# Kernel tuning notes

Hardware: AMD Instinct MI355X
Metric: run time of the kernel (lower is better)

## Reference

```python
import jax, jax.numpy as jnp
from jax import lax
import numpy as np

B, GRID, H = 128, 28, 64      # batch, 28x28 pixel grid, hidden size
NDIR = 4                      # feature_sz = number of scan directions
FC_HD, OUT = 512, 10


def setup_inputs() -> dict:
    key = jax.random.key(0)
    ks = jax.random.split(key, 8)
    s_u = 1.0 / np.sqrt(2 * H)
    inp = {
        "x":  jax.random.normal(ks[0], (B, GRID, GRID), dtype=jnp.float32),
        # per-direction MDLSTM gate params: 5 gates (i, f_left, f_up, o, g)
        "Wx": jax.random.normal(ks[1], (NDIR, 5 * H), dtype=jnp.float32) * 0.1,
        "U":  jax.random.normal(ks[2], (NDIR, 2 * H, 5 * H), dtype=jnp.float32) * s_u,
        "b":  jnp.zeros((NDIR, 5 * H), dtype=jnp.float32),
        # fc head
        "W1": jax.random.normal(ks[3], (NDIR * H, FC_HD), dtype=jnp.float32) / np.sqrt(NDIR * H),
        "b1": jnp.zeros((FC_HD,), dtype=jnp.float32),
        "W2": jax.random.normal(ks[4], (FC_HD, OUT), dtype=jnp.float32) / np.sqrt(FC_HD),
        "b2": jnp.zeros((OUT,), dtype=jnp.float32),
    }
    return inp


def _mdlstm_dir(xg, Wx, U, b):
    # xg: [GRID(rows), GRID(cols), B] scalar pixel per cell
    zeros = jnp.zeros((xg.shape[-1], H), dtype=xg.dtype)

    def col_step(carry, inp):
        h_left, c_left = carry
        x_pix, h_up, c_up = inp                     # [B], [B,H], [B,H]
        z = x_pix[:, None] * Wx + jnp.concatenate([h_left, h_up], -1) @ U + b
        i, f1, f2, o, g = jnp.split(z, 5, axis=-1)  # each [B,H]
        c = (jax.nn.sigmoid(i) * jnp.tanh(g)
             + jax.nn.sigmoid(f1) * c_left
             + jax.nn.sigmoid(f2) * c_up)
        h = jax.nn.sigmoid(o) * jnp.tanh(c)
        return (h, c), (h, c)

    def row_step(carry, x_row):
        h_up_row, c_up_row = carry                  # [GRID,B,H] previous row
        _, (h_row, c_row) = lax.scan(col_step, (zeros, zeros),
                                     (x_row, h_up_row, c_up_row))
        return (h_row, c_row), None

    init = (jnp.zeros((GRID,) + zeros.shape, xg.dtype),
            jnp.zeros((GRID,) + zeros.shape, xg.dtype))
    (h_last_row, _), _ = lax.scan(row_step, init, xg)
    return h_last_row[-1]                           # final (bottom-right) hidden [B,H]


def _forward(x, Wx, U, b, W1, b1, W2, b2):
    x2 = x.reshape(-1, GRID, GRID)
    # 4 scan directions via flips; scan always proceeds top-left -> bottom-right
    dirs = jnp.stack([x2,
                      x2[:, :, ::-1],
                      x2[:, ::-1, :],
                      x2[:, ::-1, ::-1]], 0)        # [4,B,GRID,GRID]
    dirs = jnp.transpose(dirs, (0, 2, 3, 1))        # [4,GRID,GRID,B]
    h = jax.vmap(_mdlstm_dir)(dirs, Wx, U, b)       # [4,B,H]
    h = jnp.transpose(h, (1, 0, 2)).reshape(-1, NDIR * H)
    z = jax.nn.relu(h @ W1 + b1)
    return jax.nn.softmax(z @ W2 + b2, axis=-1)


def reference(x, Wx, U, b, W1, b1, W2, b2):
    return _forward(x, Wx, U, b, W1, b1, W2, b2)
```

## Files before the change

kernel.cpp:

```cpp
#include <hip/hip_runtime.h>
#include <hip/hip_bf16.h>


#define GRIDN 28
#define BATCH 128
#define HID   64
#define NDIR  4
#define FC_HD 512
#define OUT_N 10
#define BT    2
#define NTHR  768
#define NSLOT 29
#define S_H   104
#define S_C   68

typedef _Float16 f16;
typedef _Float16 f16x8 __attribute__((ext_vector_type(8)));
typedef float    f32x4 __attribute__((ext_vector_type(4)));

__device__ __forceinline__ float sigf(float x) {
    return __builtin_amdgcn_rcpf(1.0f + __expf(-x));
}
__device__ __forceinline__ float tanh_fast(float x) {
    return 1.0f - 2.0f * __builtin_amdgcn_rcpf(1.0f + __expf(2.0f * x));
}

__global__ __launch_bounds__(NTHR)
void mdlstm_kernel(const float* __restrict__ x,
                   const float* __restrict__ Wx,
                   const float* __restrict__ U,
                   const float* __restrict__ bias,
                   float* __restrict__ Hout)
{
    const int d    = blockIdx.x & 3;
    const int tile = blockIdx.x >> 2;
    const int tid  = threadIdx.x;
    const int lane = tid & 63;
    const int wave = tid >> 6;
    const int wm   = wave >> 2;
    const int wh   = wave & 3;
    const int l16  = lane & 15;
    const int q    = lane >> 4;
    const int nb   = wh * 16 + l16;

    __shared__ __align__(16) f16 Fh[2][BT][NSLOT * S_H];
    __shared__ float             Fc[2][BT][NSLOT * S_C];
    __shared__ float             xs[GRIDN][GRIDN][BT];

    for (int i = tid; i < 2 * BT * NSLOT * S_H; i += NTHR) ((f16*)Fh)[i] = (f16)0.0f;
    for (int i = tid; i < 2 * BT * NSLOT * S_C; i += NTHR) ((float*)Fc)[i] = 0.0f;
    for (int i = tid; i < GRIDN * GRIDN * BT; i += NTHR) {
        int bl = i & 1, rc = i >> 1, c = rc % GRIDN, r = rc / GRIDN;
        int rr = (d & 2) ? (GRIDN - 1 - r) : r;
        int cc = (d & 1) ? (GRIDN - 1 - c) : c;
        xs[r][c][bl] = x[((tile * BT + bl) * GRIDN + rr) * GRIDN + cc];
    }

    f16x8 bf[5][5];
#pragma unroll
    for (int g = 0; g < 5; ++g) {
        int n = g * 64 + nb;
#pragma unroll
        for (int ks = 0; ks < 4; ++ks) {
            f16x8 v;
            int kb = ks * 32 + q * 8;
#pragma unroll
            for (int j = 0; j < 8; ++j)
                v[j] = (f16)U[(d * 128 + kb + j) * 320 + n];
            bf[g][ks] = v;
        }
        f16x8 v5 = {(f16)0, (f16)0, (f16)0, (f16)0, (f16)0, (f16)0, (f16)0, (f16)0};
        if (q == 0) {
            v5[0] = (f16)Wx[d * 320 + n];
            v5[1] = (f16)bias[d * 320 + n];
        }
        bf[g][4] = v5;
    }
    __syncthreads();

    if (tid < 2 * BT * NSLOT) {
        int buf = tid / (BT * NSLOT), rem = tid % (BT * NSLOT);
        int b = rem / NSLOT, sl = rem % NSLOT;
        Fh[buf][b][sl * S_H + 65] = (f16)1.0f;
    }
    if (tid < BT) Fh[0][tid][27 * S_H + 64] = (f16)xs[0][0][tid];
    __syncthreads();

    for (int t = 0; t < 2 * GRIDN - 1; ++t) {
        const int rlo = (t > GRIDN - 1) ? (t - (GRIDN - 1)) : 0;
        const int rhi = (t < GRIDN - 1) ? t : (GRIDN - 1);
        const int k   = rhi - rlo + 1;
        const int nM  = (2 * k + 15) >> 4;
        const int br  = t & 1, bw = br ^ 1;

        if (t < 2 * GRIDN - 2 && tid >= NTHR - 56) {
            int idx = tid - (NTHR - 56), b = idx & 1, j = idx >> 1;
            int rlo2 = (t + 1 > GRIDN - 1) ? (t + 1 - (GRIDN - 1)) : 0;
            int rhi2 = (t + 1 < GRIDN - 1) ? (t + 1) : (GRIDN - 1);
            if (j <= rhi2 - rlo2) {
                int r = rlo2 + j;
                Fh[bw][b][(27 - r) * S_H + 64] = (f16)xs[r][t + 1 - r][b];
            }
        }

        for (int mt = wm; mt < nM; mt += 3) {
            int mA = mt * 16 + l16;
            int jA = mA >> 1; if (jA > k - 1) jA = k - 1;
            int bA = mA & 1;
            int slA = 27 - (rlo + jA);
            const f16* ab = &Fh[br][bA][slA * S_H];
            f16x8 a0 = *(const f16x8*)(ab + q * 8);
            f16x8 a1 = *(const f16x8*)(ab + 32 + q * 8);
            f16x8 a2 = *(const f16x8*)(ab + S_H + q * 8);
            f16x8 a3 = *(const f16x8*)(ab + S_H + 32 + q * 8);
            f16x8 a4 = *(const f16x8*)(ab + 64 + q * 8);

            f32x4 acc[5];
#pragma unroll
            for (int g = 0; g < 5; ++g) acc[g] = (f32x4){0.f, 0.f, 0.f, 0.f};
#pragma unroll
            for (int g = 0; g < 5; ++g) acc[g] = __builtin_amdgcn_mfma_f32_16x16x32_f16(a0, bf[g][0], acc[g], 0, 0, 0);
#pragma unroll
            for (int g = 0; g < 5; ++g) acc[g] = __builtin_amdgcn_mfma_f32_16x16x32_f16(a1, bf[g][1], acc[g], 0, 0, 0);
#pragma unroll
            for (int g = 0; g < 5; ++g) acc[g] = __builtin_amdgcn_mfma_f32_16x16x32_f16(a2, bf[g][2], acc[g], 0, 0, 0);
#pragma unroll
            for (int g = 0; g < 5; ++g) acc[g] = __builtin_amdgcn_mfma_f32_16x16x32_f16(a3, bf[g][3], acc[g], 0, 0, 0);
#pragma unroll
            for (int g = 0; g < 5; ++g) acc[g] = __builtin_amdgcn_mfma_f32_16x16x32_f16(a4, bf[g][4], acc[g], 0, 0, 0);

            int j0  = mt * 8 + q * 2;
            int jj0 = (j0     > k - 1) ? k - 1 : j0;
            int jj1 = (j0 + 1 > k - 1) ? k - 1 : j0 + 1;
            int sl0 = 27 - (rlo + jj0);
            int sl1 = 27 - (rlo + jj1);
#pragma unroll
            for (int i = 0; i < 4; ++i) {
                int  b  = i & 1;
                int  sl = (i < 2) ? sl0 : sl1;
                float cl = Fc[br][b][sl * S_C + nb];
                float cu = Fc[br][b][(sl + 1) * S_C + nb];
                float ig = sigf(acc[0][i]);
                float f1 = sigf(acc[1][i]);
                float f2 = sigf(acc[2][i]);
                float og = sigf(acc[3][i]);
                float gg = tanh_fast(acc[4][i]);
                float cn = ig * gg + f1 * cl + f2 * cu;
                float hn = og * tanh_fast(cn);
                Fc[bw][b][sl * S_C + nb] = cn;
                Fh[bw][b][sl * S_H + nb] = (f16)hn;
            }
        }
        __syncthreads();
    }

    if (tid < BT * HID) {
        int bl = tid >> 6, h = tid & 63;
        Hout[(d * BATCH + tile * BT + bl) * HID + h] = (float)Fh[1][bl][h];
    }
}

__global__ __launch_bounds__(256)
void fc_kernel(const float* __restrict__ Hin,
               const float* __restrict__ W1, const float* __restrict__ b1,
               const float* __restrict__ W2, const float* __restrict__ b2,
               float* __restrict__ out)
{
    const int b   = blockIdx.x;
    const int tid = threadIdx.x;
    __shared__ float hrow[NDIR * HID];
    __shared__ float z1[FC_HD];
    __shared__ float ps[16][16];
    __shared__ float z2[16];

    hrow[tid] = Hin[(tid >> 6) * (BATCH * HID) + b * HID + (tid & 63)];
    __syncthreads();

    {
        float s0 = b1[tid], s1 = b1[tid + 256];
#pragma unroll 8
        for (int f = 0; f < NDIR * HID; ++f) {
            float h = hrow[f];
            s0 += h * W1[f * FC_HD + tid];
            s1 += h * W1[f * FC_HD + tid + 256];
        }
        z1[tid]       = fmaxf(s0, 0.0f);
        z1[tid + 256] = fmaxf(s1, 0.0f);
    }
    __syncthreads();

    {
        int j = tid & 15, sl = tid >> 4;
        float s = 0.0f;
        if (j < OUT_N) {
#pragma unroll
            for (int i = 0; i < 32; ++i) {
                int kk = sl * 32 + i;
                s += z1[kk] * W2[kk * OUT_N + j];
            }
        }
        ps[sl][j] = s;
    }
    __syncthreads();

    if (tid < OUT_N) {
        float s = b2[tid];
#pragma unroll
        for (int sl = 0; sl < 16; ++sl) s += ps[sl][tid];
        z2[tid] = s;
    }
    __syncthreads();

    if (tid == 0) {
        float m = z2[0];
        for (int j = 1; j < OUT_N; ++j) m = fmaxf(m, z2[j]);
        float sum = 0.0f, e[OUT_N];
        for (int j = 0; j < OUT_N; ++j) { e[j] = __expf(z2[j] - m); sum += e[j]; }
        float inv = 1.0f / sum;
        for (int j = 0; j < OUT_N; ++j) out[b * OUT_N + j] = e[j] * inv;
    }
}

extern "C" void kernel_launch(void* const* d_in, const int* in_sizes, int n_in,
                              void* d_out, int out_size, void* d_ws, size_t ws_size,
                              hipStream_t stream) {
    const float* x  = (const float*)d_in[0];
    const float* Wx = (const float*)d_in[1];
    const float* U  = (const float*)d_in[2];
    const float* bs = (const float*)d_in[3];
    const float* W1 = (const float*)d_in[4];
    const float* b1 = (const float*)d_in[5];
    const float* W2 = (const float*)d_in[6];
    const float* b2 = (const float*)d_in[7];
    float* out = (float*)d_out;
    float* Hws = (float*)d_ws;

    mdlstm_kernel<<<NDIR * (BATCH / BT), NTHR, 0, stream>>>(x, Wx, U, bs, Hws);
    fc_kernel<<<BATCH, 256, 0, stream>>>(Hws, W1, b1, W2, b2, out);
}
```

Baseline: 169.3 us.

## Fold exp scaling into weights, cut to 8 waves, unroll wavefront by buffer parity

After: 154.5 us. 1.1x faster.

```diff
diff --git a/kernel.cpp b/kernel.cpp
--- a/kernel.cpp
+++ b/kernel.cpp
@@ -9,7 +9,7 @@
 #define FC_HD 512
 #define OUT_N 10
 #define BT    2
-#define NTHR  768
+#define NTHR  512
 #define NSLOT 29
 #define S_H   104
 #define S_C   68
@@ -18,11 +18,13 @@
 typedef _Float16 f16x8 __attribute__((ext_vector_type(8)));
 typedef float    f32x4 __attribute__((ext_vector_type(4)));
 
-__device__ __forceinline__ float sigf(float x) {
-    return __builtin_amdgcn_rcpf(1.0f + __expf(-x));
-}
-__device__ __forceinline__ float tanh_fast(float x) {
-    return 1.0f - 2.0f * __builtin_amdgcn_rcpf(1.0f + __expf(2.0f * x));
+#define LOG2E  1.44269504088896340736f
+#define LOG2E2 2.88539008177792681472f
+
+__device__ __forceinline__ float rcpf(float x) { return __builtin_amdgcn_rcpf(x); }
+__device__ __forceinline__ float ex2(float x)  { return __builtin_amdgcn_exp2f(x); }
+__device__ __forceinline__ float tanh_c(float x) {
+    return 1.0f - 2.0f * rcpf(1.0f + ex2(LOG2E2 * x));
 }
 
 __global__ __launch_bounds__(NTHR)
@@ -59,6 +61,7 @@
     f16x8 bf[5][5];
 #pragma unroll
     for (int g = 0; g < 5; ++g) {
+        const float sc = (g == 4) ? LOG2E2 : -LOG2E;
         int n = g * 64 + nb;
 #pragma unroll
         for (int ks = 0; ks < 4; ++ks) {
@@ -66,13 +69,13 @@
             int kb = ks * 32 + q * 8;
 #pragma unroll
             for (int j = 0; j < 8; ++j)
-                v[j] = (f16)U[(d * 128 + kb + j) * 320 + n];
+                v[j] = (f16)(sc * U[(d * 128 + kb + j) * 320 + n]);
             bf[g][ks] = v;
         }
         f16x8 v5 = {(f16)0, (f16)0, (f16)0, (f16)0, (f16)0, (f16)0, (f16)0, (f16)0};
         if (q == 0) {
-            v5[0] = (f16)Wx[d * 320 + n];
-            v5[1] = (f16)bias[d * 320 + n];
+            v5[0] = (f16)(sc * Wx[d * 320 + n]);
+            v5[1] = (f16)(sc * bias[d * 320 + n]);
         }
         bf[g][4] = v5;
     }
@@ -86,12 +89,12 @@
     if (tid < BT) Fh[0][tid][27 * S_H + 64] = (f16)xs[0][0][tid];
     __syncthreads();
 
-    for (int t = 0; t < 2 * GRIDN - 1; ++t) {
+    auto step = [&](int t, int br) __attribute__((always_inline)) {
+        const int bw  = br ^ 1;
         const int rlo = (t > GRIDN - 1) ? (t - (GRIDN - 1)) : 0;
         const int rhi = (t < GRIDN - 1) ? t : (GRIDN - 1);
         const int k   = rhi - rlo + 1;
         const int nM  = (2 * k + 15) >> 4;
-        const int br  = t & 1, bw = br ^ 1;
 
         if (t < 2 * GRIDN - 2 && tid >= NTHR - 56) {
             int idx = tid - (NTHR - 56), b = idx & 1, j = idx >> 1;
@@ -103,7 +106,7 @@
             }
         }
 
-        for (int mt = wm; mt < nM; mt += 3) {
+        for (int mt = wm; mt < nM; mt += 2) {
             int mA = mt * 16 + l16;
             int jA = mA >> 1; if (jA > k - 1) jA = k - 1;
             int bA = mA & 1;
@@ -115,9 +118,10 @@
             f16x8 a3 = *(const f16x8*)(ab + S_H + 32 + q * 8);
             f16x8 a4 = *(const f16x8*)(ab + 64 + q * 8);
 
+            const f32x4 z4 = {0.f, 0.f, 0.f, 0.f};
             f32x4 acc[5];
 #pragma unroll
-            for (int g = 0; g < 5; ++g) acc[g] = (f32x4){0.f, 0.f, 0.f, 0.f};
+            for (int g = 0; g < 5; ++g) acc[g] = __builtin_amdgcn_mfma_f32_16x16x32_f16(a4, bf[g][4], z4, 0, 0, 0);
 #pragma unroll
             for (int g = 0; g < 5; ++g) acc[g] = __builtin_amdgcn_mfma_f32_16x16x32_f16(a0, bf[g][0], acc[g], 0, 0, 0);
 #pragma unroll
@@ -126,33 +130,39 @@
             for (int g = 0; g < 5; ++g) acc[g] = __builtin_amdgcn_mfma_f32_16x16x32_f16(a2, bf[g][2], acc[g], 0, 0, 0);
 #pragma unroll
             for (int g = 0; g < 5; ++g) acc[g] = __builtin_amdgcn_mfma_f32_16x16x32_f16(a3, bf[g][3], acc[g], 0, 0, 0);
-#pragma unroll
-            for (int g = 0; g < 5; ++g) acc[g] = __builtin_amdgcn_mfma_f32_16x16x32_f16(a4, bf[g][4], acc[g], 0, 0, 0);
 
             int j0  = mt * 8 + q * 2;
             int jj0 = (j0     > k - 1) ? k - 1 : j0;
             int jj1 = (j0 + 1 > k - 1) ? k - 1 : j0 + 1;
             int sl0 = 27 - (rlo + jj0);
             int sl1 = 27 - (rlo + jj1);
+
+            const float* rp[4] = { &Fc[br][0][sl0 * S_C + nb], &Fc[br][1][sl0 * S_C + nb],
+                                   &Fc[br][0][sl1 * S_C + nb], &Fc[br][1][sl1 * S_C + nb] };
+            const int DC = (bw - br) * (BT * NSLOT * S_C);
+            int ih0 = sl0 * S_H + nb, ih1 = sl1 * S_H + nb;
+            f16* wh0 = &Fh[bw][0][0];
+            f16* wh1 = &Fh[bw][1][0];
 #pragma unroll
             for (int i = 0; i < 4; ++i) {
-                int  b  = i & 1;
-                int  sl = (i < 2) ? sl0 : sl1;
-                float cl = Fc[br][b][sl * S_C + nb];
-                float cu = Fc[br][b][(sl + 1) * S_C + nb];
-                float ig = sigf(acc[0][i]);
-                float f1 = sigf(acc[1][i]);
-                float f2 = sigf(acc[2][i]);
-                float og = sigf(acc[3][i]);
-                float gg = tanh_fast(acc[4][i]);
+                float cl = rp[i][0];
+                float cu = rp[i][S_C];
+                float ig = rcpf(1.0f + ex2(acc[0][i]));
+                float f1 = rcpf(1.0f + ex2(acc[1][i]));
+                float f2 = rcpf(1.0f + ex2(acc[2][i]));
+                float og = rcpf(1.0f + ex2(acc[3][i]));
+                float gg = 1.0f - 2.0f * rcpf(1.0f + ex2(acc[4][i]));
                 float cn = ig * gg + f1 * cl + f2 * cu;
-                float hn = og * tanh_fast(cn);
-                Fc[bw][b][sl * S_C + nb] = cn;
-                Fh[bw][b][sl * S_H + nb] = (f16)hn;
+                float hn = og * tanh_c(cn);
+                *(float*)(rp[i] + DC) = cn;
+                ((i & 1) ? wh1 : wh0)[(i < 2) ? ih0 : ih1] = (f16)hn;
             }
         }
         __syncthreads();
-    }
+    };
+
+    for (int tb = 0; tb < 27; ++tb) { step(2 * tb, 0); step(2 * tb + 1, 1); }
+    step(54, 0);
 
     if (tid < BT * HID) {
         int bl = tid >> 6, h = tid & 63;
```
